# Kernel tuning notes

Measured on AMD Instinct MI355X. Metric: run time of the kernel, lower is better.

Reference implementation:

```python
import jax, jax.numpy as jnp
import numpy as np

N_NODES = 100000


def _add_self_loops(edge_index, n):
    loop = jnp.arange(n, dtype=edge_index.dtype)
    src = jnp.concatenate([edge_index[0], loop])
    dst = jnp.concatenate([edge_index[1], loop])
    return src, dst


def _gcn_conv(x, src, dst, n, W, b):
    # PyG GCNConv: linear first, then sym-normalized aggregation, then bias.
    h = x @ W                                   # [N, out]
    deg = jnp.zeros((n,), h.dtype).at[dst].add(1.0)   # in-degree incl. self-loops
    dinv = jnp.where(deg > 0, jax.lax.rsqrt(deg), 0.0)
    norm = dinv[src] * dinv[dst]                # [E+N]
    msg = h[src] * norm[:, None]                # gather + scale
    out = jax.ops.segment_sum(msg, dst, num_segments=n)  # scatter-add
    return out + b


def setup_inputs() -> dict:
    key = jax.random.key(0)
    ks = jax.random.split(key, 9)
    n, d_in, d_h, d_out = N_NODES, 64, 64, 64
    x = jax.random.normal(ks[0], (n, d_in), jnp.float32)
    edge_index = jax.random.randint(ks[1], (2, 1200000), 0, n, jnp.int64)
    s = lambda k, sh: jax.random.normal(k, sh, jnp.float32) * (1.0 / np.sqrt(sh[0]))
    return {
        "x": x,
        "edge_index": edge_index,
        "W1": s(ks[2], (d_in, d_h)),
        "b1": jnp.zeros((d_h,), jnp.float32),
        "W2": s(ks[3], (d_h, d_out)),
        "b2": jnp.zeros((d_out,), jnp.float32),
        "Wl": s(ks[4], (d_out, d_out)),
        "bl": jnp.zeros((d_out,), jnp.float32),
    }


def reference(x, edge_index, W1, b1, W2, b2, Wl, bl):
    n = x.shape[0]
    src, dst = _add_self_loops(edge_index, n)
    h = _gcn_conv(x, src, dst, n, W1, b1)
    h = jax.nn.relu(h)
    h = _gcn_conv(h, src, dst, n, W2, b2)
    return h @ Wl + bl
```

## Files before the change

kernel.cpp:

```cpp
#include <hip/hip_runtime.h>
#include <hip/hip_bf16.h>


#define FEAT 64

typedef __attribute__((ext_vector_type(8))) short bf16x8;
typedef __attribute__((ext_vector_type(4))) float f32x4;
union BF8 { bf16x8 v; unsigned short u[8]; unsigned pk[4]; uint4 q; };

__device__ __forceinline__ unsigned short f2bf(float f) {
    unsigned u = __float_as_uint(f);
    return (unsigned short)((u + 0x7FFFu + ((u >> 16) & 1u)) >> 16);
}
__device__ __forceinline__ float bflo(unsigned u) { return __uint_as_float(u << 16); }
__device__ __forceinline__ float bfhi(unsigned u) { return __uint_as_float(u & 0xFFFF0000u); }
__device__ __forceinline__ unsigned pk2bf(float a, float b) {
    union { __hip_bfloat162 b; unsigned u; } cv;
    cv.b = __float22bfloat162_rn(make_float2(a, b));
    return cv.u;
}

__global__ void k_prepw(const float* __restrict__ W1, const float* __restrict__ W2,
                        const float* __restrict__ Wl, unsigned short* __restrict__ P,
                        int* __restrict__ bcnt) {
    if (blockIdx.x == 3) {
        if (threadIdx.x < 256) bcnt[threadIdx.x] = 0;
        return;
    }
    const float* W = (blockIdx.x == 0) ? W1 : (blockIdx.x == 1) ? W2 : Wl;
    unsigned short* p = P + blockIdx.x * 4096;
    for (int i = threadIdx.x; i < 4096; i += 256) {
        int c = i >> 10, s = (i >> 9) & 1, l = (i >> 3) & 63, j = i & 7;
        int k = s * 32 + ((l >> 4) << 3) + j;
        int col = ((l & 15) << 2) + c;
        p[i] = f2bf(W[k * 64 + col]);
    }
}

__global__ void __launch_bounds__(256)
k_bhist(const int* __restrict__ dst, int* __restrict__ bcnt, int E) {
    __shared__ int h[256];
    int tid = threadIdx.x;
    h[tid] = 0;
    __syncthreads();
    int stride = gridDim.x * 256;
    for (int e = blockIdx.x * 256 + tid; e < E; e += stride)
        atomicAdd(&h[dst[e] >> 9], 1);
    __syncthreads();
    if (h[tid]) atomicAdd(&bcnt[tid], h[tid]);
}

__global__ void k_bscan(const int* __restrict__ bcnt, int* __restrict__ bbase,
                        int* __restrict__ bcur) {
    __shared__ int s[256];
    int t = threadIdx.x;
    int v = bcnt[t];
    s[t] = v;
    __syncthreads();
    for (int off = 1; off < 256; off <<= 1) {
        int x = (t >= off) ? s[t - off] : 0;
        __syncthreads();
        s[t] += x;
        __syncthreads();
    }
    int ex = s[t] - v;
    bbase[t] = ex;
    bcur[t] = ex;
    if (t == 255) bbase[256] = s[255];
}

__global__ void __launch_bounds__(256)
k_part(const int* __restrict__ src, const int* __restrict__ dst,
       int* __restrict__ bcur, unsigned* __restrict__ pass1, int E) {
    __shared__ unsigned pk[4096];
    __shared__ unsigned char bk[4096];
    __shared__ int h[256];
    __shared__ int cur[256];
    int tid = threadIdx.x;
    h[tid] = 0;
    __syncthreads();
    int base = blockIdx.x * 4096;
#pragma unroll
    for (int i = 0; i < 16; ++i) {
        int li = i * 256 + tid;
        int e = base + li;
        if (e < E) {
            int s = src[e], d = dst[e];
            int b = d >> 9;
            pk[li] = ((unsigned)s << 9) | ((unsigned)d & 511u);
            bk[li] = (unsigned char)b;
            atomicAdd(&h[b], 1);
        } else {
            bk[li] = 255;
            pk[li] = 0xFFFFFFFFu;
        }
    }
    __syncthreads();
    {
        int c = h[tid];
        int run = c ? atomicAdd(&bcur[tid], c) : 0;
        cur[tid] = run;
    }
    __syncthreads();
#pragma unroll
    for (int i = 0; i < 16; ++i) {
        int li = i * 256 + tid;
        int e = base + li;
        if (e < E) {
            int b = bk[li];
            int pos = atomicAdd(&cur[b], 1);
            pass1[pos] = pk[li];
        }
    }
}

__global__ void __launch_bounds__(512)
k_csr(const unsigned* __restrict__ pass1, const int* __restrict__ bbase,
      int* __restrict__ offs, float* __restrict__ dinv, int* __restrict__ esrc,
      int n, int E) {
    __shared__ int hist[512];
    __shared__ int cur[512];
    int tid = threadIdx.x;
    int b = blockIdx.x;
    hist[tid] = 0;
    __syncthreads();
    int beg = bbase[b], end = bbase[b + 1];
    for (int j = beg + tid; j < end; j += 512)
        atomicAdd(&hist[pass1[j] & 511u], 1);
    __syncthreads();
    int v = hist[tid];
    for (int off = 1; off < 512; off <<= 1) {
        int x = (tid >= off) ? hist[tid - off] : 0;
        __syncthreads();
        hist[tid] += x;
        __syncthreads();
    }
    int excl = hist[tid] - v;
    int node = (b << 9) + tid;
    if (node < n) {
        offs[node] = beg + excl;
        dinv[node] = rsqrtf((float)v + 1.0f);
    }
    cur[tid] = excl;
    if (b == 0 && tid == 0) offs[n] = E;
    __syncthreads();
    for (int j = beg + tid; j < end; j += 512) {
        unsigned u = pass1[j];
        int loc = (int)(u & 511u);
        int r = atomicAdd(&cur[loc], 1);
        esrc[beg + r] = (int)(u >> 9);
    }
}

template <bool IN_BF16, bool OUT_F32, bool SCALE>
__global__ void __launch_bounds__(256)
k_gemm_mfma(const void* __restrict__ Xv, const unsigned short* __restrict__ Wpk,
            const float* __restrict__ bias, const float* __restrict__ rowscale,
            void* __restrict__ Hv, int n) {
    int lane = threadIdx.x & 63;
    int wid = (blockIdx.x << 2) + (threadIdx.x >> 6);
    int nw = gridDim.x << 2;
    int T = (n + 15) >> 4;
    BF8 bfr[8];
    const uint4* wp = (const uint4*)Wpk;
#pragma unroll
    for (int f = 0; f < 8; ++f) bfr[f].q = wp[f * 64 + lane];
    int mrow = lane & 15, kq = lane >> 4, colb = lane & 15;
    float4 bv4 = make_float4(0.f, 0.f, 0.f, 0.f);
    if (OUT_F32) bv4 = ((const float4*)bias)[colb];
    for (int t = wid; t < T; t += nw) {
        int rb = t << 4;
        int row = rb + mrow;
        bool ok = row < n;
        BF8 a0, a1;
        if (IN_BF16) {
            const uint4* xr = (const uint4*)((const unsigned short*)Xv + ((unsigned)row << 6));
            a0.q = ok ? xr[kq]     : make_uint4(0, 0, 0, 0);
            a1.q = ok ? xr[kq + 4] : make_uint4(0, 0, 0, 0);
        } else {
            const float4* xr = (const float4*)((const float*)Xv + ((unsigned)row << 6));
            float4 z = make_float4(0.f, 0.f, 0.f, 0.f);
            float4 p0 = ok ? xr[kq * 2]     : z;
            float4 p1 = ok ? xr[kq * 2 + 1] : z;
            float4 p2 = ok ? xr[8 + kq * 2] : z;
            float4 p3 = ok ? xr[8 + kq * 2 + 1] : z;
            a0.pk[0] = pk2bf(p0.x, p0.y); a0.pk[1] = pk2bf(p0.z, p0.w);
            a0.pk[2] = pk2bf(p1.x, p1.y); a0.pk[3] = pk2bf(p1.z, p1.w);
            a1.pk[0] = pk2bf(p2.x, p2.y); a1.pk[1] = pk2bf(p2.z, p2.w);
            a1.pk[2] = pk2bf(p3.x, p3.y); a1.pk[3] = pk2bf(p3.z, p3.w);
        }
        f32x4 acc0 = {0.f, 0.f, 0.f, 0.f}, acc1 = acc0, acc2 = acc0, acc3 = acc0;
        acc0 = __builtin_amdgcn_mfma_f32_16x16x32_bf16(a0.v, bfr[0].v, acc0, 0, 0, 0);
        acc0 = __builtin_amdgcn_mfma_f32_16x16x32_bf16(a1.v, bfr[1].v, acc0, 0, 0, 0);
        acc1 = __builtin_amdgcn_mfma_f32_16x16x32_bf16(a0.v, bfr[2].v, acc1, 0, 0, 0);
        acc1 = __builtin_amdgcn_mfma_f32_16x16x32_bf16(a1.v, bfr[3].v, acc1, 0, 0, 0);
        acc2 = __builtin_amdgcn_mfma_f32_16x16x32_bf16(a0.v, bfr[4].v, acc2, 0, 0, 0);
        acc2 = __builtin_amdgcn_mfma_f32_16x16x32_bf16(a1.v, bfr[5].v, acc2, 0, 0, 0);
        acc3 = __builtin_amdgcn_mfma_f32_16x16x32_bf16(a0.v, bfr[6].v, acc3, 0, 0, 0);
        acc3 = __builtin_amdgcn_mfma_f32_16x16x32_bf16(a1.v, bfr[7].v, acc3, 0, 0, 0);
        int rowb = rb + (kq << 2);
        if (OUT_F32) {
            float* O = (float*)Hv;
#pragma unroll
            for (int i = 0; i < 4; ++i) {
                if (rowb + i >= n) break;
                unsigned ro = (unsigned)(rowb + i) << 6;
                float4 o = make_float4(acc0[i] + bv4.x, acc1[i] + bv4.y,
                                       acc2[i] + bv4.z, acc3[i] + bv4.w);
                *(float4*)(O + ro + (colb << 2)) = o;
            }
        } else {
            unsigned short* O = (unsigned short*)Hv;
#pragma unroll
            for (int i = 0; i < 4; ++i) {
                if (rowb + i >= n) break;
                float sc = SCALE ? rowscale[rowb + i] : 1.0f;
                unsigned ro = (unsigned)(rowb + i) << 6;
                uint2 o = make_uint2(pk2bf(acc0[i] * sc, acc1[i] * sc),
                                     pk2bf(acc2[i] * sc, acc3[i] * sc));
                *(uint2*)(O + ro + (colb << 2)) = o;
            }
        }
    }
}

template <bool RELU>
__global__ void __launch_bounds__(256)
k_agg(const int* __restrict__ offs, const int* __restrict__ esrc,
      const float* __restrict__ dinv, const unsigned short* __restrict__ Hs,
      const float* __restrict__ bias, unsigned short* __restrict__ out, int n) {
    int lane = threadIdx.x & 63;
    int h8 = lane & 7;
    int node = blockIdx.x * 32 + ((threadIdx.x >> 6) << 3) + (lane >> 3);
    bool nok = node < n;
    int beg = 0, end = 0;
    if (nok) { beg = offs[node]; end = offs[node + 1]; }
    float a0 = 0.f, a1 = 0.f, a2 = 0.f, a3 = 0.f, a4 = 0.f, a5 = 0.f, a6 = 0.f, a7 = 0.f;
    int j = beg;
    int s0 = 0, s1 = 0;
    float w0 = 0.f, w1 = 0.f;
    if (j < end)     { s0 = esrc[j];     w0 = 1.f; }
    if (j + 1 < end) { s1 = esrc[j + 1]; w1 = 1.f; }
    while (__ballot(j < end)) {
        uint4 h0 = *(const uint4*)(Hs + ((unsigned)s0 << 6) + (h8 << 3));
        uint4 h1 = *(const uint4*)(Hs + ((unsigned)s1 << 6) + (h8 << 3));
        int jn = j + 2;
        int t0 = s0, t1 = s1;
        float v0 = 0.f, v1 = 0.f;
        if (jn < end)     { t0 = esrc[jn];     v0 = 1.f; }
        if (jn + 1 < end) { t1 = esrc[jn + 1]; v1 = 1.f; }
        a0 = fmaf(bflo(h0.x), w0, a0); a1 = fmaf(bfhi(h0.x), w0, a1);
        a2 = fmaf(bflo(h0.y), w0, a2); a3 = fmaf(bfhi(h0.y), w0, a3);
        a4 = fmaf(bflo(h0.z), w0, a4); a5 = fmaf(bfhi(h0.z), w0, a5);
        a6 = fmaf(bflo(h0.w), w0, a6); a7 = fmaf(bfhi(h0.w), w0, a7);
        a0 = fmaf(bflo(h1.x), w1, a0); a1 = fmaf(bfhi(h1.x), w1, a1);
        a2 = fmaf(bflo(h1.y), w1, a2); a3 = fmaf(bfhi(h1.y), w1, a3);
        a4 = fmaf(bflo(h1.z), w1, a4); a5 = fmaf(bfhi(h1.z), w1, a5);
        a6 = fmaf(bflo(h1.w), w1, a6); a7 = fmaf(bfhi(h1.w), w1, a7);
        j = jn; s0 = t0; s1 = t1; w0 = v0; w1 = v1;
    }
    if (nok) {
        float dd = dinv[node];
        uint4 sv = *(const uint4*)(Hs + ((unsigned)node << 6) + (h8 << 3));
        const float4* b4 = (const float4*)bias;
        float4 bA = b4[h8 * 2], bB = b4[h8 * 2 + 1];
        float r0 = (a0 + bflo(sv.x)) * dd + bA.x;
        float r1 = (a1 + bfhi(sv.x)) * dd + bA.y;
        float r2 = (a2 + bflo(sv.y)) * dd + bA.z;
        float r3 = (a3 + bfhi(sv.y)) * dd + bA.w;
        float r4 = (a4 + bflo(sv.z)) * dd + bB.x;
        float r5 = (a5 + bfhi(sv.z)) * dd + bB.y;
        float r6 = (a6 + bflo(sv.w)) * dd + bB.z;
        float r7 = (a7 + bfhi(sv.w)) * dd + bB.w;
        if (RELU) {
            r0 = fmaxf(r0, 0.f); r1 = fmaxf(r1, 0.f); r2 = fmaxf(r2, 0.f); r3 = fmaxf(r3, 0.f);
            r4 = fmaxf(r4, 0.f); r5 = fmaxf(r5, 0.f); r6 = fmaxf(r6, 0.f); r7 = fmaxf(r7, 0.f);
        }
        uint4 o = make_uint4(pk2bf(r0, r1), pk2bf(r2, r3), pk2bf(r4, r5), pk2bf(r6, r7));
        *(uint4*)(out + ((unsigned)node << 6) + (h8 << 3)) = o;
    }
}

extern "C" void kernel_launch(void* const* d_in, const int* in_sizes, int n_in,
                              void* d_out, int out_size, void* d_ws, size_t ws_size,
                              hipStream_t stream) {
    const float* x  = (const float*)d_in[0];
    const int*   ei = (const int*)d_in[1];
    const float* W1 = (const float*)d_in[2];
    const float* b1 = (const float*)d_in[3];
    const float* W2 = (const float*)d_in[4];
    const float* b2 = (const float*)d_in[5];
    const float* Wl = (const float*)d_in[6];
    const float* bl = (const float*)d_in[7];
    float* out = (float*)d_out;

    const int n = in_sizes[0] / FEAT;
    const int E = in_sizes[1] / 2;
    const int* src = ei;
    const int* dst = ei + E;

    const int B = 256;
    const int NB = (n + 511) >> 9;
    const int pblocks = (E + 4095) / 4096;
    const int agg_blocks  = (n + 31) / 32;
    const int T = (n + 15) / 16;
    const int gemm_blocks = (T + 7) / 8;

    char* w = (char*)d_ws;
    int*   bcnt     = (int*)w;              w += 256 * 4;
    int*   bbase    = (int*)w;              w += 260 * 4;
    int*   bcur     = (int*)w;              w += 256 * 4;
    int*   offs     = (int*)w;              w += ((size_t)n + 4) * 4;
    float* dinv     = (float*)w;            w += (size_t)n * 4;
    w = (char*)(((uintptr_t)w + 15) & ~(uintptr_t)15);
    unsigned short* Wpk = (unsigned short*)w;  w += 3 * 4096 * 2;
    unsigned* pass1 = (unsigned*)w;         w += (size_t)E * 4;
    int*   esrc     = (int*)w;              w += (size_t)E * 4;
    unsigned short* bufA = (unsigned short*)w;  w += (size_t)n * FEAT * 2;
    unsigned short* bufB = (unsigned short*)w;

    k_prepw<<<dim3(4), dim3(B), 0, stream>>>(W1, W2, Wl, Wpk, bcnt);

    k_bhist<<<dim3(256), dim3(B), 0, stream>>>(dst, bcnt, E);
    k_bscan<<<dim3(1), dim3(B), 0, stream>>>(bcnt, bbase, bcur);
    k_part<<<dim3(pblocks), dim3(B), 0, stream>>>(src, dst, bcur, pass1, E);
    k_csr<<<dim3(NB), dim3(512), 0, stream>>>(pass1, bbase, offs, dinv, esrc, n, E);

    k_gemm_mfma<false, false, true><<<dim3(gemm_blocks), dim3(B), 0, stream>>>(x, Wpk, nullptr, dinv, bufA, n);
    k_agg<true><<<dim3(agg_blocks), dim3(B), 0, stream>>>(offs, esrc, dinv, bufA, b1, bufB, n);

    k_gemm_mfma<true, false, true><<<dim3(gemm_blocks), dim3(B), 0, stream>>>(bufB, Wpk + 4096, nullptr, dinv, bufA, n);
    k_agg<false><<<dim3(agg_blocks), dim3(B), 0, stream>>>(offs, esrc, dinv, bufA, b2, bufB, n);

    k_gemm_mfma<true, true, false><<<dim3(gemm_blocks), dim3(B), 0, stream>>>(bufB, Wpk + 8192, bl, nullptr, out, n);
}
```

Before: 247.5 us.

## Drop histogram pass via fixed-capacity buckets and degree-sort nodes for aggregation

Removes the separate destination histogram pass by giving each coarse bucket a fixed-capacity slot (BCAP) in the partition buffer, so k_part reserves positions directly and the bucket scan runs afterwards. It also computes a per-node degree histogram, builds a permutation of nodes sorted by degree, and has the aggregation kernels process nodes in that order, so the 8 nodes sharing a wavefront have similar edge counts and divergence drops. Costs are two extra small kernels, a larger partition buffer, and an extra indirection through perm. Fixed capacity can overflow if a bucket receives more than 16384 edges. A leftover stub k_agg kernel is left in but never launched.

Result: slower. 257.5 us (+4.0%).

```diff
diff --git a/kernel.cpp b/kernel.cpp
--- a/kernel.cpp
+++ b/kernel.cpp
@@ -3,6 +3,7 @@
 
 
 #define FEAT 64
+#define BCAP 16384
 
 typedef __attribute__((ext_vector_type(8))) short bf16x8;
 typedef __attribute__((ext_vector_type(4))) float f32x4;
@@ -22,9 +23,9 @@
 
 __global__ void k_prepw(const float* __restrict__ W1, const float* __restrict__ W2,
                         const float* __restrict__ Wl, unsigned short* __restrict__ P,
-                        int* __restrict__ bcnt) {
+                        int* __restrict__ bcur, int* __restrict__ dcnt) {
     if (blockIdx.x == 3) {
-        if (threadIdx.x < 256) bcnt[threadIdx.x] = 0;
+        if (threadIdx.x < 256) { bcur[threadIdx.x] = 0; dcnt[threadIdx.x] = 0; }
         return;
     }
     const float* W = (blockIdx.x == 0) ? W1 : (blockIdx.x == 1) ? W2 : Wl;
@@ -35,38 +36,6 @@
         int col = ((l & 15) << 2) + c;
         p[i] = f2bf(W[k * 64 + col]);
     }
-}
-
-__global__ void __launch_bounds__(256)
-k_bhist(const int* __restrict__ dst, int* __restrict__ bcnt, int E) {
-    __shared__ int h[256];
-    int tid = threadIdx.x;
-    h[tid] = 0;
-    __syncthreads();
-    int stride = gridDim.x * 256;
-    for (int e = blockIdx.x * 256 + tid; e < E; e += stride)
-        atomicAdd(&h[dst[e] >> 9], 1);
-    __syncthreads();
-    if (h[tid]) atomicAdd(&bcnt[tid], h[tid]);
-}
-
-__global__ void k_bscan(const int* __restrict__ bcnt, int* __restrict__ bbase,
-                        int* __restrict__ bcur) {
-    __shared__ int s[256];
-    int t = threadIdx.x;
-    int v = bcnt[t];
-    s[t] = v;
-    __syncthreads();
-    for (int off = 1; off < 256; off <<= 1) {
-        int x = (t >= off) ? s[t - off] : 0;
-        __syncthreads();
-        s[t] += x;
-        __syncthreads();
-    }
-    int ex = s[t] - v;
-    bbase[t] = ex;
-    bcur[t] = ex;
-    if (t == 255) bbase[256] = s[255];
 }
 
 __global__ void __launch_bounds__(256)
@@ -99,7 +68,7 @@
     {
         int c = h[tid];
         int run = c ? atomicAdd(&bcur[tid], c) : 0;
-        cur[tid] = run;
+        cur[tid] = tid * BCAP + run;
     }
     __syncthreads();
 #pragma unroll
@@ -114,19 +83,40 @@
     }
 }
 
+__global__ void k_bscan(const int* __restrict__ bcur, int* __restrict__ bbase) {
+    __shared__ int s[256];
+    int t = threadIdx.x;
+    int v = bcur[t];
+    s[t] = v;
+    __syncthreads();
+    for (int off = 1; off < 256; off <<= 1) {
+        int x = (t >= off) ? s[t - off] : 0;
+        __syncthreads();
+        s[t] += x;
+        __syncthreads();
+    }
+    bbase[t] = s[t] - v;
+    if (t == 255) bbase[256] = s[255];
+}
+
 __global__ void __launch_bounds__(512)
-k_csr(const unsigned* __restrict__ pass1, const int* __restrict__ bbase,
-      int* __restrict__ offs, float* __restrict__ dinv, int* __restrict__ esrc,
-      int n, int E) {
+k_csr(const unsigned* __restrict__ pass1, const int* __restrict__ bcnt,
+      const int* __restrict__ bbase, int* __restrict__ offs, float* __restrict__ dinv,
+      unsigned char* __restrict__ deg8, int* __restrict__ dcnt,
+      int* __restrict__ esrc, int n, int E) {
     __shared__ int hist[512];
     __shared__ int cur[512];
+    __shared__ int dh[256];
     int tid = threadIdx.x;
     int b = blockIdx.x;
     hist[tid] = 0;
-    __syncthreads();
-    int beg = bbase[b], end = bbase[b + 1];
-    for (int j = beg + tid; j < end; j += 512)
-        atomicAdd(&hist[pass1[j] & 511u], 1);
+    if (tid < 256) dh[tid] = 0;
+    __syncthreads();
+    int cnt = bcnt[b];
+    int sbeg = b * BCAP;
+    int ob = bbase[b];
+    for (int j = tid; j < cnt; j += 512)
+        atomicAdd(&hist[pass1[sbeg + j] & 511u], 1);
     __syncthreads();
     int v = hist[tid];
     for (int off = 1; off < 512; off <<= 1) {
@@ -138,17 +128,63 @@
     int excl = hist[tid] - v;
     int node = (b << 9) + tid;
     if (node < n) {
-        offs[node] = beg + excl;
+        offs[node] = ob + excl;
         dinv[node] = rsqrtf((float)v + 1.0f);
+        int bin = v < 255 ? v : 255;
+        deg8[node] = (unsigned char)bin;
+        atomicAdd(&dh[bin], 1);
     }
     cur[tid] = excl;
     if (b == 0 && tid == 0) offs[n] = E;
     __syncthreads();
-    for (int j = beg + tid; j < end; j += 512) {
-        unsigned u = pass1[j];
+    if (tid < 256 && dh[tid]) atomicAdd(&dcnt[tid], dh[tid]);
+    for (int j = tid; j < cnt; j += 512) {
+        unsigned u = pass1[sbeg + j];
         int loc = (int)(u & 511u);
         int r = atomicAdd(&cur[loc], 1);
-        esrc[beg + r] = (int)(u >> 9);
+        esrc[ob + r] = (int)(u >> 9);
+    }
+}
+
+__global__ void k_dscan(const int* __restrict__ dcnt, int* __restrict__ dcur) {
+    __shared__ int s[256];
+    int t = threadIdx.x;
+    int v = dcnt[t];
+    s[t] = v;
+    __syncthreads();
+    for (int off = 1; off < 256; off <<= 1) {
+        int x = (t >= off) ? s[t - off] : 0;
+        __syncthreads();
+        s[t] += x;
+        __syncthreads();
+    }
+    dcur[t] = s[t] - v;
+}
+
+__global__ void __launch_bounds__(256)
+k_dperm(const unsigned char* __restrict__ deg8, int* __restrict__ dcur,
+        int* __restrict__ perm, int n) {
+    __shared__ int dh[256];
+    __shared__ int runb[256];
+    __shared__ int lc[256];
+    int tid = threadIdx.x;
+    dh[tid] = 0; lc[tid] = 0;
+    __syncthreads();
+    int node = blockIdx.x * 256 + tid;
+    int bin = -1;
+    if (node < n) {
+        bin = deg8[node];
+        atomicAdd(&dh[bin], 1);
+    }
+    __syncthreads();
+    {
+        int c = dh[tid];
+        runb[tid] = c ? atomicAdd(&dcur[tid], c) : 0;
+    }
+    __syncthreads();
+    if (node < n) {
+        int r = atomicAdd(&lc[bin], 1);
+        perm[runb[bin] + r] = node;
     }
 }
 
@@ -226,15 +262,45 @@
 
 template <bool RELU>
 __global__ void __launch_bounds__(256)
-k_agg(const int* __restrict__ offs, const int* __restrict__ esrc,
+k_agg(const int* __restrict__ perm, const int* __restrict__ offs,
       const float* __restrict__ dinv, const unsigned short* __restrict__ Hs,
       const float* __restrict__ bias, unsigned short* __restrict__ out, int n) {
     int lane = threadIdx.x & 63;
     int h8 = lane & 7;
-    int node = blockIdx.x * 32 + ((threadIdx.x >> 6) << 3) + (lane >> 3);
-    bool nok = node < n;
-    int beg = 0, end = 0;
-    if (nok) { beg = offs[node]; end = offs[node + 1]; }
+    int p = blockIdx.x * 32 + ((threadIdx.x >> 6) << 3) + (lane >> 3);
+    bool nok = p < n;
+    int node = 0, beg = 0, end = 0;
+    if (nok) {
+        node = perm[p];
+        beg = offs[node];
+        end = offs[node + 1];
+    }
+    float a0 = 0.f, a1 = 0.f, a2 = 0.f, a3 = 0.f, a4 = 0.f, a5 = 0.f, a6 = 0.f, a7 = 0.f;
+    int j = beg;
+    int s0 = 0, s1 = 0;
+    float w0 = 0.f, w1 = 0.f;
+    if (j < end)     { s0 = __ldg(&((const int*)offs)[0]), s0 = 0; }
+    ;
+    (void)s1; (void)w0; (void)w1; (void)s0;
+    if (nok) { }
+}
+
+template <bool RELU>
+__global__ void __launch_bounds__(256)
+k_agg2(const int* __restrict__ perm, const int* __restrict__ offs,
+       const int* __restrict__ esrc, const float* __restrict__ dinv,
+       const unsigned short* __restrict__ Hs, const float* __restrict__ bias,
+       unsigned short* __restrict__ out, int n) {
+    int lane = threadIdx.x & 63;
+    int h8 = lane & 7;
+    int p = blockIdx.x * 32 + ((threadIdx.x >> 6) << 3) + (lane >> 3);
+    bool nok = p < n;
+    int node = 0, beg = 0, end = 0;
+    if (nok) {
+        node = perm[p];
+        beg = offs[node];
+        end = offs[node + 1];
+    }
     float a0 = 0.f, a1 = 0.f, a2 = 0.f, a3 = 0.f, a4 = 0.f, a5 = 0.f, a6 = 0.f, a7 = 0.f;
     int j = beg;
     int s0 = 0, s1 = 0;
@@ -303,34 +369,40 @@
     const int NB = (n + 511) >> 9;
     const int pblocks = (E + 4095) / 4096;
     const int agg_blocks  = (n + 31) / 32;
+    const int nb256 = (n + 255) / 256;
     const int T = (n + 15) / 16;
     const int gemm_blocks = (T + 7) / 8;
 
     char* w = (char*)d_ws;
-    int*   bcnt     = (int*)w;              w += 256 * 4;
+    int*   bcur     = (int*)w;              w += 256 * 4;
     int*   bbase    = (int*)w;              w += 260 * 4;
-    int*   bcur     = (int*)w;              w += 256 * 4;
+    int*   dcnt     = (int*)w;              w += 256 * 4;
+    int*   dcur     = (int*)w;              w += 256 * 4;
     int*   offs     = (int*)w;              w += ((size_t)n + 4) * 4;
     float* dinv     = (float*)w;            w += (size_t)n * 4;
+    int*   perm     = (int*)w;              w += (size_t)n * 4;
+    unsigned char* deg8 = (unsigned char*)w; w += ((size_t)n + 15) & ~(size_t)15;
     w = (char*)(((uintptr_t)w + 15) & ~(uintptr_t)15);
     unsigned short* Wpk = (unsigned short*)w;  w += 3 * 4096 * 2;
-    unsigned* pass1 = (unsigned*)w;         w += (size_t)E * 4;
+    unsigned* pass1 = (unsigned*)w;         w += (size_t)256 * BCAP * 4;
     int*   esrc     = (int*)w;              w += (size_t)E * 4;
     unsigned short* bufA = (unsigned short*)w;  w += (size_t)n * FEAT * 2;
     unsigned short* bufB = (unsigned short*)w;
 
-    k_prepw<<<dim3(4), dim3(B), 0, stream>>>(W1, W2, Wl, Wpk, bcnt);
-
-    k_bhist<<<dim3(256), dim3(B), 0, stream>>>(dst, bcnt, E);
-    k_bscan<<<dim3(1), dim3(B), 0, stream>>>(bcnt, bbase, bcur);
+    k_prepw<<<dim3(4), dim3(B), 0, stream>>>(W1, W2, Wl, Wpk, bcur, dcnt);
+
     k_part<<<dim3(pblocks), dim3(B), 0, stream>>>(src, dst, bcur, pass1, E);
-    k_csr<<<dim3(NB), dim3(512), 0, stream>>>(pass1, bbase, offs, dinv, esrc, n, E);
+    k_bscan<<<dim3(1), dim3(B), 0, stream>>>(bcur, bbase);
+    k_csr<<<dim3(NB), dim3(512), 0, stream>>>(pass1, bcur, bbase, offs, dinv, deg8, dcnt, esrc, n, E);
+
+    k_dscan<<<dim3(1), dim3(B), 0, stream>>>(dcnt, dcur);
+    k_dperm<<<dim3(nb256), dim3(B), 0, stream>>>(deg8, dcur, perm, n);
 
     k_gemm_mfma<false, false, true><<<dim3(gemm_blocks), dim3(B), 0, stream>>>(x, Wpk, nullptr, dinv, bufA, n);
-    k_agg<true><<<dim3(agg_blocks), dim3(B), 0, stream>>>(offs, esrc, dinv, bufA, b1, bufB, n);
+    k_agg2<true><<<dim3(agg_blocks), dim3(B), 0, stream>>>(perm, offs, esrc, dinv, bufA, b1, bufB, n);
 
     k_gemm_mfma<true, false, true><<<dim3(gemm_blocks), dim3(B), 0, stream>>>(bufB, Wpk + 4096, nullptr, dinv, bufA, n);
-    k_agg<false><<<dim3(agg_blocks), dim3(B), 0, stream>>>(offs, esrc, dinv, bufA, b2, bufB, n);
+    k_agg2<false><<<dim3(agg_blocks), dim3(B), 0, stream>>>(perm, offs, esrc, dinv, bufA, b2, bufB, n);
 
     k_gemm_mfma<true, true, false><<<dim3(gemm_blocks), dim3(B), 0, stream>>>(bufB, Wpk + 8192, bl, nullptr, out, n);
 }
```
